# Kernel optimization log

Hardware: AMD Instinct MI355X
Metric: run time of the kernel (lower is better)

## Reference

```python
import jax, jax.numpy as jnp
import numpy as np

KMAX = 192  # static upper bound on sampled subset size k (E[k]~116, std~10 for our vals)


def _dpp_sample(vals, vecs, seed):
    """Sequential DPP sampling (Hough et al. algorithm), jit-compatible via
    fixed-width column padding (KMAX) and lax.while_loop over the k iterations.
    The original's nested classical Gram-Schmidt re-orthonormalization is
    expressed as a QR factorization with the R-diagonal sign convention of GS."""
    n = vals.shape[0]
    key = jax.random.key(seed)
    k_idx, k_loop = jax.random.split(key)

    # Bernoulli selection of eigenvectors: rand(n) < vals/(vals+1)
    index = jax.random.uniform(k_idx, (n,)) < vals / (vals + 1.0)
    k = jnp.sum(index.astype(jnp.int32))
    kk = jnp.minimum(k, KMAX)

    # Pack selected eigenvector columns to the left (stable sort: True first)
    order = jnp.argsort(~index)
    colmask0 = (jnp.arange(KMAX) < kk).astype(vals.dtype)
    V0 = vecs[:, order[:KMAX]] * colmask0[None, :]  # [n, KMAX]

    cols = jnp.arange(KMAX)

    def cond(st):
        i, V, subset = st
        return i < kk

    def body(st):
        i, V, subset = st
        m = kk - i  # number of active columns
        # p_i = ||V[i,:]||^2 over active columns (inactive cols are zero)
        p = jnp.sum(V * V, axis=1)
        c = jnp.cumsum(p / jnp.sum(p))
        u = jax.random.uniform(jax.random.fold_in(k_loop, i))
        item = jnp.argmax(u < c)  # first index where cdf exceeds u
        subset = subset.at[item].set(jnp.asarray(1.0, subset.dtype))
        # first active column j with |V[item, j]| > 0
        jmask = (jnp.abs(V[item]) > 0) & (cols < m)
        j = jnp.argmax(jmask)
        Vj = V[:, j]
        # delete column j (shift left), shrink active width to m-1
        src = jnp.minimum(jnp.where(cols >= j, cols + 1, cols), KMAX - 1)
        newmask = (cols < (m - 1)).astype(V.dtype)
        Vd = V[:, src] * newmask[None, :]
        # eliminate: V <- V - Vj * V[item,:] / Vj[item]
        Ve = (Vd - jnp.outer(Vj, Vd[item] / Vj[item])) * newmask[None, :]
        # re-orthonormalize active columns (classical GS == QR with positive R diag)
        Q, R = jnp.linalg.qr(Ve)
        d = jnp.diagonal(R)
        Q = Q * jnp.where(d >= 0, 1.0, -1.0)[None, :]
        Vn = Q * newmask[None, :]
        Vn = jnp.where(m > 1, Vn, V)  # original skips update when V has 1 column
        return (i + 1, Vn, subset)

    subset0 = jnp.zeros((n,), vals.dtype)
    _, _, subset = jax.lax.while_loop(cond, body, (jnp.int32(0), V0, subset0))
    # original returns all-ones when every eigenvector is selected
    return jnp.where(k == n, jnp.ones((n,), vals.dtype), subset)


def setup_inputs() -> dict:
    key = jax.random.key(0)
    k1, k2 = jax.random.split(key)
    n = 2048
    # eigenvalues in (0.01, 0.11) so E[|subset|] ~ 0.054*n ~ 116 << KMAX
    e = jax.random.uniform(k1, (n,), jnp.float32) * 0.1 + 0.01
    # orthonormal eigenvectors (proper eigendecomposition of a DPP kernel)
    v = jnp.linalg.qr(jax.random.normal(k2, (n, n), jnp.float32))[0]
    return {"e": e, "v": v, "seed": 0}


def reference(e, v, seed):
    return _dpp_sample(e, v, seed)
```

## Files before the change

kernel.cpp:

```cpp
#include <hip/hip_runtime.h>
#include <hip/hip_fp16.h>
#include <stdint.h>
#include <stddef.h>

#define N 2048
#define KMX 192
#define NTH 1024

typedef _Float16 f16x2 __attribute__((ext_vector_type(2)));
typedef _Float16 f16x4 __attribute__((ext_vector_type(4)));

#if defined(__has_builtin)
#if __has_builtin(__builtin_amdgcn_fdot2)
#define HAS_FDOT2 1
#endif
#endif

__device__ __forceinline__ f16x2 bch2(unsigned u) { return __builtin_bit_cast(f16x2, u); }
__device__ __forceinline__ unsigned packh2(float a, float b) {
  unsigned ua = (unsigned)__half_as_ushort(__float2half(a));
  unsigned ub = (unsigned)__half_as_ushort(__float2half(b));
  return ua | (ub << 16);
}
__device__ __forceinline__ float dot2acc(unsigned c, unsigned y, float acc) {
#ifdef HAS_FDOT2
  return __builtin_amdgcn_fdot2(bch2(c), bch2(y), acc, false);
#else
  f16x2 cv = bch2(c), yv = bch2(y);
  acc = fmaf((float)cv[0], (float)yv[0], acc);
  acc = fmaf((float)cv[1], (float)yv[1], acc);
  return acc;
#endif
}

__device__ __forceinline__ void tfround(unsigned &x0, unsigned &x1, const int d) {
  x0 += x1;
  x1 = (x1 << d) | (x1 >> (32 - d));
  x1 ^= x0;
}

__device__ __forceinline__ uint2 tf2x32(unsigned k0, unsigned k1, unsigned c0, unsigned c1) {
  unsigned ks2 = k0 ^ k1 ^ 0x1BD11BDAu;
  unsigned x0 = c0 + k0, x1 = c1 + k1;
  tfround(x0,x1,13); tfround(x0,x1,15); tfround(x0,x1,26); tfround(x0,x1,6);
  x0 += k1;  x1 += ks2 + 1u;
  tfround(x0,x1,17); tfround(x0,x1,29); tfround(x0,x1,16); tfround(x0,x1,24);
  x0 += ks2; x1 += k0 + 2u;
  tfround(x0,x1,13); tfround(x0,x1,15); tfround(x0,x1,26); tfround(x0,x1,6);
  x0 += k0;  x1 += k1 + 3u;
  tfround(x0,x1,17); tfround(x0,x1,29); tfround(x0,x1,16); tfround(x0,x1,24);
  x0 += k1;  x1 += ks2 + 4u;
  tfround(x0,x1,13); tfround(x0,x1,15); tfround(x0,x1,26); tfround(x0,x1,6);
  x0 += ks2; x1 += k0 + 5u;
  uint2 r; r.x = x0; r.y = x1;
  return r;
}

__device__ __forceinline__ float u01(unsigned bits) {
  return __uint_as_float((bits >> 9) | 0x3f800000u) - 1.0f;
}

__global__ void k_select(const float* __restrict__ e, const int* __restrict__ seedp,
                         int* __restrict__ hdr, int* __restrict__ sel) {
  __shared__ unsigned kx0, kx1;
  __shared__ int cnt_s[256];
  __shared__ int pre_s[256];
  const int tid = threadIdx.x;
  if (tid == 0) {
    unsigned seed = (unsigned)seedp[0];
    uint2 kidx  = tf2x32(0u, seed, 0u, 0u);
    uint2 kloop = tf2x32(0u, seed, 0u, 1u);
    kx0 = kidx.x; kx1 = kidx.y;
    hdr[2] = (int)kloop.x;
    hdr[3] = (int)kloop.y;
  }
  __syncthreads();
  const unsigned a0 = kx0, a1 = kx1;
  int flags = 0;
  #pragma unroll
  for (int r = 0; r < 8; ++r) {
    const int i = tid * 8 + r;
    uint2 o = tf2x32(a0, a1, 0u, (unsigned)i);
    float u = u01(o.x ^ o.y);
    float ev = e[i];
    float thr = ev / (ev + 1.0f);
    if (u < thr) flags |= (1 << r);
  }
  cnt_s[tid] = __popc(flags);
  __syncthreads();
  if (tid == 0) {
    int acc = 0;
    for (int t2 = 0; t2 < 256; ++t2) { pre_s[t2] = acc; acc += cnt_s[t2]; }
    hdr[1] = acc;
    hdr[0] = acc < KMX ? acc : KMX;
  }
  __syncthreads();
  int off = pre_s[tid];
  #pragma unroll
  for (int r = 0; r < 8; ++r) {
    if (flags & (1 << r)) {
      if (off < KMX) sel[off] = tid * 8 + r;
      ++off;
    }
  }
}

__global__ void k_gather_h(const float* __restrict__ v, const int* __restrict__ hdr,
                           const int* __restrict__ sel, __half* __restrict__ Gh) {
  const int j = blockIdx.y;
  const int i = blockIdx.x * 256 + threadIdx.x;
  float val = 0.f;
  if (j < hdr[0]) val = v[(size_t)i * N + sel[j]];
  Gh[j * N + i] = __float2half(val);
}

__global__ void k_gather(const float* __restrict__ v, const int* __restrict__ hdr,
                         const int* __restrict__ sel, float* __restrict__ G,
                         __half* __restrict__ Gh) {
  const int j = blockIdx.y;
  const int i = blockIdx.x * 256 + threadIdx.x;
  float val = 0.f;
  if (j < hdr[0]) val = v[(size_t)i * N + sel[j]];
  G[j * N + i] = val;
  Gh[j * N + i] = __float2half(val);
}

__global__ void __launch_bounds__(256)
k_gram(const __half* __restrict__ Gh, const int* __restrict__ hdr,
       __half* __restrict__ Kh) {
  __shared__ __align__(16) __half As[32][64];
  __shared__ __align__(16) __half Bs[32][64];
  const int tid = threadIdx.x;
  const int i0 = blockIdx.y * 64;
  const int i1 = blockIdx.x * 64;
  const int tr = tid & 15, tc = tid >> 4;
  const int kk = hdr[0];
  int kc = (kk + 31) & ~31;
  if (kc > KMX) kc = KMX;

  float acc[4][4];
  #pragma unroll
  for (int r = 0; r < 4; ++r)
    #pragma unroll
    for (int c = 0; c < 4; ++c) acc[r][c] = 0.f;

  const int jr = tid >> 3, c8 = (tid & 7) * 8;
  for (int j0 = 0; j0 < kc; j0 += 32) {
    *(uint4*)&As[jr][c8] = *(const uint4*)(Gh + (size_t)(j0 + jr) * N + i0 + c8);
    *(uint4*)&Bs[jr][c8] = *(const uint4*)(Gh + (size_t)(j0 + jr) * N + i1 + c8);
    __syncthreads();
    #pragma unroll 8
    for (int k = 0; k < 32; ++k) {
      f16x4 a4 = *(const f16x4*)&As[k][tr * 4];
      f16x4 b4 = *(const f16x4*)&Bs[k][tc * 4];
      #pragma unroll
      for (int r = 0; r < 4; ++r)
        #pragma unroll
        for (int c = 0; c < 4; ++c)
          acc[r][c] = fmaf((float)a4[r], (float)b4[c], acc[r][c]);
    }
    __syncthreads();
  }
  #pragma unroll
  for (int r = 0; r < 4; ++r) {
    const int row = i0 + tr * 4 + r;
    uint2 w;
    w.x = packh2(acc[r][0], acc[r][1]);
    w.y = packh2(acc[r][2], acc[r][3]);
    *(uint2*)(Kh + (size_t)row * N + i1 + tc * 4) = w;
  }
}

__global__ void __launch_bounds__(NTH)
k_dpp_chol(const int* __restrict__ hdr, const __half* __restrict__ Kh,
           uint2* __restrict__ YQ, float* __restrict__ out) {
  __shared__ float p_s[N];
  __shared__ uint2 cpack_s[KMX / 4];
  __shared__ float u_s[KMX];
  __shared__ float wsum_s[16];
  __shared__ float rinv_sh;
  __shared__ int item_sh;

  const int tid  = threadIdx.x;
  const int lane = tid & 63;
  const int wave = tid >> 6;
  const int kk    = hdr[0];
  const int kfull = hdr[1];
  const unsigned kl0 = (unsigned)hdr[2];
  const unsigned kl1 = (unsigned)hdr[3];

  const float fill = (kfull == N) ? 1.0f : 0.0f;
  out[tid] = fill;
  out[tid + NTH] = fill;
  if (kfull == N || kk == 0) return;

  {
    const int i0 = 2 * tid;
    p_s[i0]     = (float)Kh[(size_t)i0 * N + i0];
    p_s[i0 + 1] = (float)Kh[(size_t)(i0 + 1) * N + i0 + 1];
    if (tid < KMX) {
      uint2 fk = tf2x32(kl0, kl1, 0u, (unsigned)tid);
      uint2 ob = tf2x32(fk.x, fk.y, 0u, 0u);
      u_s[tid] = u01(ob.x ^ ob.y);
    }
    if (tid == 0) item_sh = N;
  }
  __syncthreads();

  for (int t = 0; t < kk; ++t) {
    float a  = p_s[2 * tid];
    float b  = p_s[2 * tid + 1];
    float ts = a + b;
    float ws = ts;
    #pragma unroll
    for (int d = 1; d < 64; d <<= 1) {
      float o = __shfl_up(ws, d, 64);
      if (lane >= d) ws += o;
    }
    if (lane == 63) wsum_s[wave] = ws;
    __syncthreads();
    float S = 0.f, base_wave = 0.f;
    #pragma unroll
    for (int w = 0; w < 16; ++w) {
      float wv = wsum_s[w];
      if (w < wave) base_wave += wv;
      S += wv;
    }
    const float Sinv = 1.0f / S;
    const float u = u_s[t];
    float excl = __shfl_up(ws, 1, 64);
    if (lane == 0) excl = 0.f;
    const float base = base_wave + excl;
    const float c0 = (base + a) * Sinv;
    const float c1 = (base + ts) * Sinv;
    const bool m0 = (u < c0);
    const bool m1 = (u < c1);
    unsigned long long bal = __ballot(m0 || m1);
    if (bal) {
      int first = (int)__builtin_ctzll(bal);
      if (lane == first) atomicMin(&item_sh, m0 ? 2 * tid : 2 * tid + 1);
    }
    __syncthreads();
    int item = item_sh;
    if (item >= N) item = 0;
    if (tid == 0) out[item] = 1.0f;
    if (t == kk - 1) break;

    if (tid * 4 < t) {
      uint2 cu = YQ[(size_t)tid * N + item];
      cu.x ^= 0x80008000u;
      cu.y ^= 0x80008000u;
      const int rem = t - 4 * tid;
      if (rem < 4) {
        if (rem == 1)      { cu.x &= 0x0000FFFFu; cu.y = 0u; }
        else if (rem == 2) { cu.y = 0u; }
        else               { cu.y &= 0x0000FFFFu; }
      }
      cpack_s[tid] = cu;
    }
    if (tid == 0) {
      rinv_sh = 1.0f / sqrtf(fmaxf(p_s[item], 1e-30f));
      item_sh = N;
    }
    __syncthreads();

    {
      const float rinv = rinv_sh;
      const int nq = (t + 3) >> 2;
      unsigned kp = *(const unsigned*)(Kh + (size_t)item * N + 2 * tid);
      f16x2 kv = bch2(kp);
      float acc0 = (float)kv[0], acc1 = (float)kv[1];
      const uint2* Yp = YQ + 2 * tid;
      #pragma unroll 2
      for (int q = 0; q < nq; ++q) {
        uint2 cs = cpack_s[q];
        uint4 yv = *(const uint4*)(Yp + (size_t)q * N);
        acc0 = dot2acc(cs.x, yv.x, acc0);
        acc0 = dot2acc(cs.y, yv.y, acc0);
        acc1 = dot2acc(cs.x, yv.z, acc1);
        acc1 = dot2acc(cs.y, yv.w, acc1);
      }
      float y0 = acc0 * rinv, y1 = acc1 * rinv;
      p_s[2 * tid]     = fmaxf(p_s[2 * tid]     - y0 * y0, 0.f);
      p_s[2 * tid + 1] = fmaxf(p_s[2 * tid + 1] - y1 * y1, 0.f);
      unsigned short* Ys = (unsigned short*)YQ;
      const size_t eb = ((size_t)(t >> 2) * N + 2 * tid) * 4;
      Ys[eb + (t & 3)]     = __half_as_ushort(__float2half(y0));
      Ys[eb + 4 + (t & 3)] = __half_as_ushort(__float2half(y1));
    }
  }
}

__global__ void __launch_bounds__(NTH)
k_dpp_main(const int* __restrict__ hdr, const float* __restrict__ G,
           const __half* __restrict__ Gh, float* __restrict__ D,
           float* __restrict__ out) {
  __shared__ float p_s[N];
  __shared__ float g_s[KMX];
  __shared__ float part[16 * KMX];
  __shared__ float u_s[KMX];
  __shared__ float wsum_s[16];
  __shared__ int item_sh;

  const int tid  = threadIdx.x;
  const int lane = tid & 63;
  const int wave = tid >> 6;
  const int kk    = hdr[0];
  const int kfull = hdr[1];
  const unsigned kl0 = (unsigned)hdr[2];
  const unsigned kl1 = (unsigned)hdr[3];

  const float fill = (kfull == N) ? 1.0f : 0.0f;
  out[tid] = fill;
  out[tid + NTH] = fill;
  if (kfull == N || kk == 0) return;

  const int kkr = (kk + 15) & ~15;

  {
    float s0a = 0.f, s0b = 0.f, s1a = 0.f, s1b = 0.f;
    const __half* base = Gh + 2 * tid;
    for (int j = 0; j < kkr; j += 4) {
      float2 f0 = __half22float2(*(const __half2*)(base + (j + 0) * N));
      float2 f1 = __half22float2(*(const __half2*)(base + (j + 1) * N));
      float2 f2 = __half22float2(*(const __half2*)(base + (j + 2) * N));
      float2 f3 = __half22float2(*(const __half2*)(base + (j + 3) * N));
      s0a = fmaf(f0.x, f0.x, s0a); s1a = fmaf(f0.y, f0.y, s1a);
      s0b = fmaf(f1.x, f1.x, s0b); s1b = fmaf(f1.y, f1.y, s1b);
      s0a = fmaf(f2.x, f2.x, s0a); s1a = fmaf(f2.y, f2.y, s1a);
      s0b = fmaf(f3.x, f3.x, s0b); s1b = fmaf(f3.y, f3.y, s1b);
    }
    p_s[2 * tid]     = s0a + s0b;
    p_s[2 * tid + 1] = s1a + s1b;
    if (tid < KMX) {
      uint2 fk = tf2x32(kl0, kl1, 0u, (unsigned)tid);
      uint2 ob = tf2x32(fk.x, fk.y, 0u, 0u);
      u_s[tid] = u01(ob.x ^ ob.y);
    }
    if (tid == 0) item_sh = N;
  }
  __syncthreads();

  for (int t = 0; t < kk; ++t) {
    float a  = p_s[2 * tid];
    float b  = p_s[2 * tid + 1];
    float ts = a + b;
    float ws = ts;
    #pragma unroll
    for (int d = 1; d < 64; d <<= 1) {
      float o = __shfl_up(ws, d, 64);
      if (lane >= d) ws += o;
    }
    if (lane == 63) wsum_s[wave] = ws;
    __syncthreads();
    float S = 0.f, base_wave = 0.f;
    #pragma unroll
    for (int w = 0; w < 16; ++w) {
      float wv = wsum_s[w];
      if (w < wave) base_wave += wv;
      S += wv;
    }
    const float u = u_s[t];
    float excl = __shfl_up(ws, 1, 64);
    if (lane == 0) excl = 0.f;
    const float base = base_wave + excl;
    const float c0 = (base + a) / S;
    const float c1 = (base + ts) / S;
    const bool m0 = (u < c0);
    const bool m1 = (u < c1);
    unsigned long long bal = __ballot(m0 || m1);
    if (bal) {
      int first = (int)__builtin_ctzll(bal);
      if (lane == first) atomicMin(&item_sh, m0 ? 2 * tid : 2 * tid + 1);
    }
    __syncthreads();
    int item = item_sh;
    if (item >= N) item = 0;
    if (tid == 0) out[item] = 1.0f;
    if (t == kk - 1) break;

    if (tid < KMX) g_s[tid] = G[tid * N + item];
    __syncthreads();

    {
      float g0 = g_s[lane], g1 = g_s[lane + 64], g2 = g_s[lane + 128];
      float a0 = 0.f, a1 = 0.f, a2 = 0.f;
      for (int s = wave; s < t; s += 16) {
        const float* Dr = D + s * KMX;
        float d0 = Dr[lane], d1 = Dr[lane + 64], d2 = Dr[lane + 128];
        float acc = fmaf(d0, g0, fmaf(d1, g1, d2 * g2));
        #pragma unroll
        for (int m = 1; m < 64; m <<= 1) acc += __shfl_xor(acc, m, 64);
        a0 = fmaf(acc, d0, a0); a1 = fmaf(acc, d1, a1); a2 = fmaf(acc, d2, a2);
      }
      part[wave * KMX + lane]       = a0;
      part[wave * KMX + lane + 64]  = a1;
      part[wave * KMX + lane + 128] = a2;
    }
    __syncthreads();
    if (tid < KMX) {
      float gg = g_s[tid];
      #pragma unroll
      for (int w = 0; w < 16; ++w) gg -= part[w * KMX + tid];
      g_s[tid] = gg;
    }
    __syncthreads();

    float gg2 = 0.f;
    {
      float g0 = g_s[lane], g1 = g_s[lane + 64], g2 = g_s[lane + 128];
      float a0 = 0.f, a1 = 0.f, a2 = 0.f;
      for (int s = wave; s < t; s += 16) {
        const float* Dr = D + s * KMX;
        float d0 = Dr[lane], d1 = Dr[lane + 64], d2 = Dr[lane + 128];
        float acc = fmaf(d0, g0, fmaf(d1, g1, d2 * g2));
        #pragma unroll
        for (int m = 1; m < 64; m <<= 1) acc += __shfl_xor(acc, m, 64);
        a0 = fmaf(acc, d0, a0); a1 = fmaf(acc, d1, a1); a2 = fmaf(acc, d2, a2);
      }
      part[wave * KMX + lane]       = a0;
      part[wave * KMX + lane + 64]  = a1;
      part[wave * KMX + lane + 128] = a2;
    }
    __syncthreads();
    if (tid < KMX) {
      float gg = g_s[tid];
      #pragma unroll
      for (int w = 0; w < 16; ++w) gg -= part[w * KMX + tid];
      gg2 = gg;
    }
    if (wave < 3) {
      float r = gg2 * gg2;
      #pragma unroll
      for (int m = 1; m < 64; m <<= 1) r += __shfl_xor(r, m, 64);
      if (lane == 0) wsum_s[wave] = r;
    }
    __syncthreads();
    const float rho = sqrtf(wsum_s[0] + wsum_s[1] + wsum_s[2]);
    if (tid < KMX) {
      float dj = gg2 / rho;
      g_s[tid] = dj;
      D[t * KMX + tid] = dj;
    }
    if (tid == 0) item_sh = N;
    __syncthreads();

    {
      float s0a = 0.f, s0b = 0.f, s1a = 0.f, s1b = 0.f;
      const __half* base2 = Gh + 2 * tid;
      for (int j = 0; j < kkr; j += 4) {
        float d0 = g_s[j], d1 = g_s[j + 1], d2 = g_s[j + 2], d3 = g_s[j + 3];
        float2 f0 = __half22float2(*(const __half2*)(base2 + (j + 0) * N));
        float2 f1 = __half22float2(*(const __half2*)(base2 + (j + 1) * N));
        float2 f2 = __half22float2(*(const __half2*)(base2 + (j + 2) * N));
        float2 f3 = __half22float2(*(const __half2*)(base2 + (j + 3) * N));
        s0a = fmaf(f0.x, d0, s0a); s1a = fmaf(f0.y, d0, s1a);
        s0b = fmaf(f1.x, d1, s0b); s1b = fmaf(f1.y, d1, s1b);
        s0a = fmaf(f2.x, d2, s0a); s1a = fmaf(f2.y, d2, s1a);
        s0b = fmaf(f3.x, d3, s0b); s1b = fmaf(f3.y, d3, s1b);
      }
      float s0 = s0a + s0b, s1 = s1a + s1b;
      p_s[2 * tid]     = fmaxf(p_s[2 * tid]     - s0 * s0, 0.f);
      p_s[2 * tid + 1] = fmaxf(p_s[2 * tid + 1] - s1 * s1, 0.f);
    }
  }
}

extern "C" void kernel_launch(void* const* d_in, const int* in_sizes, int n_in,
                              void* d_out, int out_size, void* d_ws, size_t ws_size,
                              hipStream_t stream) {
  (void)in_sizes; (void)n_in; (void)out_size;
  const float* e    = (const float*)d_in[0];
  const float* v    = (const float*)d_in[1];
  const int*   seed = (const int*)d_in[2];
  float* out = (float*)d_out;

  int* hdr = (int*)d_ws;
  int* sel = hdr + 8;

  if (ws_size >= (size_t)12 * 1024 * 1024) {
    __half* Gh = (__half*)((char*)d_ws + 4096);
    uint2*  YQ = (uint2*)((char*)d_ws + (size_t)2560 * 1024);
    __half* Kh = (__half*)((char*)d_ws + (size_t)4096 * 1024);

    k_select<<<1, 256, 0, stream>>>(e, seed, hdr, sel);
    k_gather_h<<<dim3(8, KMX), 256, 0, stream>>>(v, hdr, sel, Gh);
    k_gram<<<dim3(32, 32), 256, 0, stream>>>(Gh, hdr, Kh);
    k_dpp_chol<<<1, NTH, 0, stream>>>(hdr, Kh, YQ, out);
  } else {
    float*  D  = (float*)((char*)d_ws + 1024);
    float*  G  = (float*)((char*)d_ws + (size_t)256 * 1024);
    __half* Gh = (__half*)((char*)d_ws + (size_t)2048 * 1024);

    k_select<<<1, 256, 0, stream>>>(e, seed, hdr, sel);
    k_gather<<<dim3(8, KMX), 256, 0, stream>>>(v, hdr, sel, G, Gh);
    k_dpp_main<<<1, NTH, 0, stream>>>(hdr, G, Gh, D, out);
  }
}
```

Baseline: 65.75 us.

## Remove a barrier per Cholesky step by double-buffering item and reading pivot row directly

Each thread now keeps its own p values in registers and computes rinv itself, instead of thread 0 publishing them through shared memory. The pivot row coefficients are read straight from global YQ rather than staged in a shared cpack buffer. The item slot is double-buffered so it can be reset without an extra barrier, which removes one __syncthreads per iteration of the sequential loop. The wave-sum prefix is done with shuffles instead of a serial 16-element loop. The cost is redundant global loads of the pivot row by every thread; these should mostly hit in cache.

```diff
diff --git a/kernel.cpp b/kernel.cpp
--- a/kernel.cpp
+++ b/kernel.cpp
@@ -175,11 +175,9 @@
 k_dpp_chol(const int* __restrict__ hdr, const __half* __restrict__ Kh,
            uint2* __restrict__ YQ, float* __restrict__ out) {
   __shared__ float p_s[N];
-  __shared__ uint2 cpack_s[KMX / 4];
   __shared__ float u_s[KMX];
   __shared__ float wsum_s[16];
-  __shared__ float rinv_sh;
-  __shared__ int item_sh;
+  __shared__ int item_sh[2];
 
   const int tid  = threadIdx.x;
   const int lane = tid & 63;
@@ -194,23 +192,22 @@
   out[tid + NTH] = fill;
   if (kfull == N || kk == 0) return;
 
-  {
-    const int i0 = 2 * tid;
-    p_s[i0]     = (float)Kh[(size_t)i0 * N + i0];
-    p_s[i0 + 1] = (float)Kh[(size_t)(i0 + 1) * N + i0 + 1];
-    if (tid < KMX) {
-      uint2 fk = tf2x32(kl0, kl1, 0u, (unsigned)tid);
-      uint2 ob = tf2x32(fk.x, fk.y, 0u, 0u);
-      u_s[tid] = u01(ob.x ^ ob.y);
-    }
-    if (tid == 0) item_sh = N;
-  }
+  const int i0 = 2 * tid;
+
+  float p0 = (float)Kh[(size_t)i0 * N + i0];
+  float p1 = (float)Kh[(size_t)(i0 + 1) * N + i0 + 1];
+  p_s[i0]     = p0;
+  p_s[i0 + 1] = p1;
+  if (tid < KMX) {
+    uint2 fk = tf2x32(kl0, kl1, 0u, (unsigned)tid);
+    uint2 ob = tf2x32(fk.x, fk.y, 0u, 0u);
+    u_s[tid] = u01(ob.x ^ ob.y);
+  }
+  if (tid == 0) { item_sh[0] = N; item_sh[1] = N; }
   __syncthreads();
 
   for (int t = 0; t < kk; ++t) {
-    float a  = p_s[2 * tid];
-    float b  = p_s[2 * tid + 1];
-    float ts = a + b;
+    float ts = p0 + p1;
     float ws = ts;
     #pragma unroll
     for (int d = 1; d < 64; d <<= 1) {
@@ -219,75 +216,77 @@
     }
     if (lane == 63) wsum_s[wave] = ws;
     __syncthreads();
-    float S = 0.f, base_wave = 0.f;
+    float wv = (lane < 16) ? wsum_s[lane] : 0.f;
     #pragma unroll
-    for (int w = 0; w < 16; ++w) {
-      float wv = wsum_s[w];
-      if (w < wave) base_wave += wv;
-      S += wv;
-    }
+    for (int d = 1; d < 16; d <<= 1) {
+      float o = __shfl_up(wv, d, 16);
+      if ((lane & 15) >= d) wv += o;
+    }
+    const float S    = __shfl(wv, 15, 64);
+    const float binc = __shfl(wv, wave, 64);
+    const float base_wave = binc - wsum_s[wave];
     const float Sinv = 1.0f / S;
     const float u = u_s[t];
     float excl = __shfl_up(ws, 1, 64);
     if (lane == 0) excl = 0.f;
     const float base = base_wave + excl;
-    const float c0 = (base + a) * Sinv;
+    const float c0 = (base + p0) * Sinv;
     const float c1 = (base + ts) * Sinv;
     const bool m0 = (u < c0);
     const bool m1 = (u < c1);
     unsigned long long bal = __ballot(m0 || m1);
     if (bal) {
       int first = (int)__builtin_ctzll(bal);
-      if (lane == first) atomicMin(&item_sh, m0 ? 2 * tid : 2 * tid + 1);
-    }
-    __syncthreads();
-    int item = item_sh;
+      if (lane == first) atomicMin(&item_sh[t & 1], m0 ? i0 : i0 + 1);
+    }
+    __syncthreads();
+    int item = item_sh[t & 1];
     if (item >= N) item = 0;
-    if (tid == 0) out[item] = 1.0f;
+    if (tid == 0) {
+      out[item] = 1.0f;
+      item_sh[(t + 1) & 1] = N;
+    }
     if (t == kk - 1) break;
 
-    if (tid * 4 < t) {
-      uint2 cu = YQ[(size_t)tid * N + item];
-      cu.x ^= 0x80008000u;
-      cu.y ^= 0x80008000u;
-      const int rem = t - 4 * tid;
-      if (rem < 4) {
-        if (rem == 1)      { cu.x &= 0x0000FFFFu; cu.y = 0u; }
-        else if (rem == 2) { cu.y = 0u; }
-        else               { cu.y &= 0x0000FFFFu; }
-      }
-      cpack_s[tid] = cu;
-    }
-    if (tid == 0) {
-      rinv_sh = 1.0f / sqrtf(fmaxf(p_s[item], 1e-30f));
-      item_sh = N;
-    }
-    __syncthreads();
-
-    {
-      const float rinv = rinv_sh;
-      const int nq = (t + 3) >> 2;
-      unsigned kp = *(const unsigned*)(Kh + (size_t)item * N + 2 * tid);
-      f16x2 kv = bch2(kp);
-      float acc0 = (float)kv[0], acc1 = (float)kv[1];
-      const uint2* Yp = YQ + 2 * tid;
-      #pragma unroll 2
-      for (int q = 0; q < nq; ++q) {
-        uint2 cs = cpack_s[q];
-        uint4 yv = *(const uint4*)(Yp + (size_t)q * N);
-        acc0 = dot2acc(cs.x, yv.x, acc0);
-        acc0 = dot2acc(cs.y, yv.y, acc0);
-        acc1 = dot2acc(cs.x, yv.z, acc1);
-        acc1 = dot2acc(cs.y, yv.w, acc1);
-      }
-      float y0 = acc0 * rinv, y1 = acc1 * rinv;
-      p_s[2 * tid]     = fmaxf(p_s[2 * tid]     - y0 * y0, 0.f);
-      p_s[2 * tid + 1] = fmaxf(p_s[2 * tid + 1] - y1 * y1, 0.f);
-      unsigned short* Ys = (unsigned short*)YQ;
-      const size_t eb = ((size_t)(t >> 2) * N + 2 * tid) * 4;
-      Ys[eb + (t & 3)]     = __half_as_ushort(__float2half(y0));
-      Ys[eb + 4 + (t & 3)] = __half_as_ushort(__float2half(y1));
-    }
+    const float pitem = p_s[item];
+    const float rinv = 1.0f / sqrtf(fmaxf(pitem, 1e-30f));
+    const int nqf = t >> 2;
+    const int rem = t & 3;
+    float acc0 = 0.f, acc1 = 0.f;
+    const uint2* Yc = YQ + item;
+    const uint2* Yp = YQ + i0;
+    #pragma unroll 2
+    for (int q = 0; q < nqf; ++q) {
+      uint2 cs = Yc[(size_t)q * N];
+      uint4 yv = *(const uint4*)(Yp + (size_t)q * N);
+      acc0 = dot2acc(cs.x, yv.x, acc0);
+      acc0 = dot2acc(cs.y, yv.y, acc0);
+      acc1 = dot2acc(cs.x, yv.z, acc1);
+      acc1 = dot2acc(cs.y, yv.w, acc1);
+    }
+    if (rem) {
+      uint2 cs = Yc[(size_t)nqf * N];
+      uint4 yv = *(const uint4*)(Yp + (size_t)nqf * N);
+      if (rem == 1)      { cs.x &= 0x0000FFFFu; cs.y = 0u; }
+      else if (rem == 2) { cs.y = 0u; }
+      else               { cs.y &= 0x0000FFFFu; }
+      acc0 = dot2acc(cs.x, yv.x, acc0);
+      acc0 = dot2acc(cs.y, yv.y, acc0);
+      acc1 = dot2acc(cs.x, yv.z, acc1);
+      acc1 = dot2acc(cs.y, yv.w, acc1);
+    }
+    unsigned kp = *(const unsigned*)(Kh + (size_t)item * N + i0);
+    f16x2 kv = bch2(kp);
+    const float y0 = ((float)kv[0] - acc0) * rinv;
+    const float y1 = ((float)kv[1] - acc1) * rinv;
+    p0 = fmaxf(p0 - y0 * y0, 0.f);
+    p1 = fmaxf(p1 - y1 * y1, 0.f);
+    p_s[i0]     = p0;
+    p_s[i0 + 1] = p1;
+    unsigned short* Ys = (unsigned short*)YQ;
+    const size_t eb = ((size_t)nqf * N + i0) * 4;
+    Ys[eb + rem]     = __half_as_ushort(__float2half(y0));
+    Ys[eb + 4 + rem] = __half_as_ushort(__float2half(y1));
   }
 }
 
```

Result: slower. 72.93 us (+10.9%).
